# Optimization experiments

Measured on AMD Instinct MI355X. Metric: run time of the kernel, lower is better.

The kernel has to match this reference:

```python
import jax, jax.numpy as jnp
import numpy as np

NUM_HEADS = 16


def setup_inputs() -> dict:
    key = jax.random.key(0)
    ks = jax.random.split(key, 8)
    S, B, E, L, P = 512, 32, 1024, 16, 10
    query = jax.random.normal(ks[0], (S, B, E), dtype=jnp.float32)
    prompt_ids = jax.random.randint(ks[1], (B, 1), 0, P, dtype=jnp.int32)
    batch_weight = jax.random.uniform(ks[2], (B,), dtype=jnp.float32)
    # xavier_uniform-like init for in_proj_weight
    bound = float(np.sqrt(6.0 / (3 * E + E)))
    in_proj_weight = jax.random.uniform(ks[3], (3 * E, E), minval=-bound, maxval=bound, dtype=jnp.float32)
    in_proj_bias = jnp.zeros((3 * E,), dtype=jnp.float32)
    ob = float(np.sqrt(6.0 / (E + E)))
    out_proj_weight = jax.random.uniform(ks[4], (E, E), minval=-ob, maxval=ob, dtype=jnp.float32)
    out_proj_bias = jnp.zeros((E,), dtype=jnp.float32)
    # prefix_pool: K-half uniform(-1,1), V-half zeros (as in torch init)
    pk = jax.random.uniform(ks[5], (P, 1, L, E), minval=-1.0, maxval=1.0, dtype=jnp.float32)
    prefix_pool = jnp.concatenate([pk, jnp.zeros((P, 1, L, E), dtype=jnp.float32)], axis=1)
    return {
        "query": query,
        "prompt_ids": prompt_ids,
        "batch_weight": batch_weight,
        "in_proj_weight": in_proj_weight,
        "in_proj_bias": in_proj_bias,
        "out_proj_weight": out_proj_weight,
        "out_proj_bias": out_proj_bias,
        "prefix_pool": prefix_pool,
    }


def _sdpa(q, k, v, scale):
    # q: [B,H,S,D], k/v: [B,H,T,D]
    scores = jnp.einsum("bhsd,bhtd->bhst", q, k) * scale
    probs = jax.nn.softmax(scores, axis=-1)
    return jnp.einsum("bhst,bhtd->bhsd", probs, v)


def reference(query, prompt_ids, batch_weight, in_proj_weight, in_proj_bias,
              out_proj_weight, out_proj_bias, prefix_pool):
    S, B, E = query.shape
    H = NUM_HEADS
    D = E // H
    scale = 1.0 / jnp.sqrt(jnp.asarray(D, dtype=query.dtype))

    # packed in-projection (q is k is v)
    qkv = query @ in_proj_weight.T + in_proj_bias          # [S,B,3E]
    q, k, v = jnp.split(qkv, 3, axis=-1)
    to_bhsd = lambda t: t.reshape(S, B, H, D).transpose(1, 2, 0, 3)  # [B,H,S,D]
    q, k, v = to_bhsd(q), to_bhsd(k), to_bhsd(v)

    # main attention
    attn = _sdpa(q, k, v, scale)                           # [B,H,S,D]

    # prefix attention
    prefix = prefix_pool[prompt_ids[:, 0]]                 # [B,2,L,E]
    L = prefix.shape[2]
    pk = prefix[:, 0].reshape(B, L, H, D).transpose(0, 2, 1, 3)  # [B,H,L,D]
    pv = prefix[:, 1].reshape(B, L, H, D).transpose(0, 2, 1, 3)
    attn_prefix = _sdpa(q, pk, pv, scale)                  # [B,H,S,D]
    attn_prefix = attn_prefix * batch_weight[:, None, None, None]

    out = attn + attn_prefix
    out = out.transpose(2, 0, 1, 3).reshape(S, B, E)       # [S,B,E]
    out = out @ out_proj_weight.T + out_proj_bias
    return out
```

## Files before the change

### kernel.cpp

```cpp
#include <hip/hip_runtime.h>
#include <stdint.h>

typedef unsigned short u16;
typedef __attribute__((ext_vector_type(8))) __bf16 bf16x8;
typedef __attribute__((ext_vector_type(4))) float f32x4;
typedef __attribute__((ext_vector_type(8))) unsigned short ushort8;

__device__ __forceinline__ u16 f2bf(float f) {
  unsigned int u = __builtin_bit_cast(unsigned int, f);
  return (u16)((u + 0x7fffu + ((u >> 16) & 1u)) >> 16);
}

__device__ __forceinline__ float fexp2(float x) {
  float r;
  asm volatile("v_exp_f32 %0, %1" : "=v"(r) : "v"(x));
  return r;
}

__device__ __forceinline__ f32x4 mfma16(bf16x8 a, bf16x8 b, f32x4 c) {
  return __builtin_amdgcn_mfma_f32_16x16x32_bf16(a, b, c, 0, 0, 0);
}

__device__ __forceinline__ void gload_lds16(const void* g, void* l) {
  __builtin_amdgcn_global_load_lds((const __attribute__((address_space(1))) void*)g,
                                   (__attribute__((address_space(3))) void*)l,
                                   16, 0, 0);
}

#define KSCALE 0.18033688011112294f

__global__ void __launch_bounds__(256) cvt_all(
    const float* __restrict__ q, const float* __restrict__ w1,
    const float* __restrict__ w2, u16* __restrict__ qb,
    u16* __restrict__ w1b, u16* __restrict__ w2b) {
  int i = blockIdx.x * 256 + threadIdx.x;
  const float* src;
  u16* dst;
  int off;
  if (i < 4194304) {
    src = q; dst = qb; off = i;
  } else if (i < 4194304 + 786432) {
    src = w1; dst = w1b; off = i - 4194304;
  } else {
    src = w2; dst = w2b; off = i - 4980736;
  }
  float4 v = ((const float4*)src)[off];
  u16* d = dst + (size_t)off * 4;
  d[0] = f2bf(v.x); d[1] = f2bf(v.y); d[2] = f2bf(v.z); d[3] = f2bf(v.w);
}

#define LDV(p) (*(const bf16x8*)(p))
#define RD_LO(AS, C) { aL[0]=LDV(AS+aRow+(C)); aL[1]=LDV(AS+aRow+1024+(C)); \
                       aL[2]=LDV(AS+aRow+2048+(C)); aL[3]=LDV(AS+aRow+3072+(C)); }
#define RD_HI(AS, C) { aH[0]=LDV(AS+aRow+4096+(C)); aH[1]=LDV(AS+aRow+5120+(C)); \
                       aH[2]=LDV(AS+aRow+6144+(C)); aH[3]=LDV(AS+aRow+7168+(C)); }
#define RD_B(BS, R, C) { R[0]=LDV(BS+bRow+(C)); R[1]=LDV(BS+bRow+1024+(C)); \
                         R[2]=LDV(BS+bRow+2048+(C)); R[3]=LDV(BS+bRow+3072+(C)); }
#define STA(DST, Q, T) gload_lds16(baseA + (Q)*K64 + (size_t)(T)*64, (DST) + (Q)*4096 + stDst)
#define STB(DST, Q, T) gload_lds16(baseB + (Q)*K64 + (size_t)(T)*64, (DST) + (Q)*4096 + stDst)
#define MM_LO(BB) { _Pragma("unroll") for (int mi=0;mi<4;++mi) \
                    _Pragma("unroll") for (int ni=0;ni<4;++ni) \
                      acc[mi][ni]=mfma16(aL[mi],(BB)[ni],acc[mi][ni]); }
#define MM_HI(BB) { _Pragma("unroll") for (int mi=0;mi<4;++mi) \
                    _Pragma("unroll") for (int ni=0;ni<4;++ni) \
                      acc[mi+4][ni]=mfma16(aH[mi],(BB)[ni],acc[mi+4][ni]); }
#define VMW(N) asm volatile("s_waitcnt vmcnt(" #N ")" ::: "memory")
#define BAR() __builtin_amdgcn_s_barrier()
#define PRIO1() __builtin_amdgcn_s_setprio(1)
#define PRIO0() __builtin_amdgcn_s_setprio(0)
#define MFMA_PH(MM, BB) { PRIO1(); MM(BB); PRIO0(); }

template <int MODE>
__global__ void __launch_bounds__(512, 2) gemm8p(
    const u16* __restrict__ A, const u16* __restrict__ B,
    const float* __restrict__ bias, void* __restrict__ Cout,
    u16* __restrict__ q_out, u16* __restrict__ k_out, u16* __restrict__ v_out,
    int M, int N, int K) {
  __shared__ alignas(16) u16 SH[65536];

  const int tid = threadIdx.x;
  const int w = tid >> 6, l = tid & 63;
  const int wm = w >> 2, wn = w & 3;
  const long bm = (long)blockIdx.x * 256;
  const long bn = (long)blockIdx.y * 256;
  const int NT = K >> 6;
  const int NIT = NT >> 1;

  const int srow = w * 8 + (l >> 3);
  const int schk = ((l & 7) ^ (l >> 3)) * 8;
  const u16* baseA = A + (bm + srow) * (size_t)K + schk;
  const u16* baseB = B + (bn + srow) * (size_t)K + schk;
  const size_t K64 = (size_t)K * 64;
  const int stDst = w * 512;

  u16* const as0 = SH;
  u16* const as1 = SH + 16384;
  u16* const bs0 = SH + 32768;
  u16* const bs1 = SH + 49152;

  const int fr = l & 15, fkg = l >> 4;
  const int sw = (fr & 7) << 3;
  const int c0 = (fkg * 8) ^ sw;
  const int c1 = (32 + fkg * 8) ^ sw;
  const int aRow = (wm * 128 + fr) * 64;
  const int bRow = (wn * 64 + fr) * 64;

  f32x4 acc[8][4] = {};
  bf16x8 aL[4], aH[4], b0[4], b1[4];

  STB(bs0, 0, 0); STB(bs0, 1, 0); STB(bs0, 2, 0); STB(bs0, 3, 0);
  STA(as0, 0, 0); STA(as0, 1, 0); STA(as0, 2, 0); STA(as0, 3, 0);
  STB(bs1, 0, 1); STB(bs1, 1, 1);
  VMW(2); BAR();
  RD_LO(as0, c0); RD_B(bs0, b0, c0);

  for (int it = 0; it < NIT - 1; ++it) {
    const int t1 = 2 * it + 1, t2 = 2 * it + 2, t3 = 2 * it + 3;
    STA(as1, 0, t1); STA(as1, 2, t1); STA(as1, 1, t1); STA(as1, 3, t1);
    STB(bs1, 2, t1); STB(bs1, 3, t1);
    RD_HI(as0, c0);
    MFMA_PH(MM_LO, b0); BAR();
    RD_LO(as0, c1); RD_B(bs0, b1, c1);
    MFMA_PH(MM_HI, b0); BAR();
    STB(bs0, 0, t2); STB(bs0, 1, t2); STB(bs0, 2, t2); STB(bs0, 3, t2);
    VMW(4);
    RD_HI(as0, c1);
    MFMA_PH(MM_LO, b1); BAR();
    STA(as0, 0, t2); STA(as0, 2, t2);
    RD_LO(as1, c0); RD_B(bs1, b0, c0);
    MFMA_PH(MM_HI, b1); BAR();
    STA(as0, 1, t2); STA(as0, 3, t2);
    RD_HI(as1, c0);
    MFMA_PH(MM_LO, b0); BAR();
    RD_LO(as1, c1); RD_B(bs1, b1, c1);
    MFMA_PH(MM_HI, b0); BAR();
    STB(bs1, 0, t3); STB(bs1, 1, t3);
    VMW(2);
    RD_HI(as1, c1);
    MFMA_PH(MM_LO, b1); BAR();
    RD_LO(as0, c0); RD_B(bs0, b0, c0);
    MFMA_PH(MM_HI, b1); BAR();
  }

  {
    const int t1 = NT - 1;
    STA(as1, 0, t1); STA(as1, 2, t1); STA(as1, 1, t1); STA(as1, 3, t1);
    STB(bs1, 2, t1); STB(bs1, 3, t1);
    RD_HI(as0, c0);
    MFMA_PH(MM_LO, b0); BAR();
    RD_LO(as0, c1); RD_B(bs0, b1, c1);
    MFMA_PH(MM_HI, b0); BAR();
    VMW(0);
    RD_HI(as0, c1);
    MFMA_PH(MM_LO, b1); BAR();
    RD_LO(as1, c0); RD_B(bs1, b0, c0);
    MFMA_PH(MM_HI, b1); BAR();
    RD_HI(as1, c0);
    MFMA_PH(MM_LO, b0); BAR();
    RD_LO(as1, c1); RD_B(bs1, b1, c1);
    MFMA_PH(MM_HI, b0); BAR();
    RD_HI(as1, c1);
    MFMA_PH(MM_LO, b1); BAR();
    MFMA_PH(MM_HI, b1);
    BAR();
  }

  if (MODE == 0) {
    const int r0 = wm * 128 + ((l >> 4) << 2);
    const int cc0 = wn * 64 + (l & 15);
#pragma unroll
    for (int mi = 0; mi < 8; ++mi) {
#pragma unroll
      for (int j = 0; j < 4; ++j) {
        long r = bm + r0 + mi * 16 + j;
#pragma unroll
        for (int ni = 0; ni < 4; ++ni) {
          long c = bn + cc0 + ni * 16;
          ((float*)Cout)[r * N + c] = acc[mi][ni][j] + bias[c];
        }
      }
    }
  } else {
    const int sec = (int)(bn >> 10);
    const float kmul = (sec == 0) ? KSCALE : 1.0f;
    const int colBase = wn * 64 + (l & 15);
    const int rowBase = wm * 128 + ((l >> 4) << 2);
#pragma unroll
    for (int mi = 0; mi < 8; ++mi) {
#pragma unroll
      for (int j = 0; j < 4; ++j) {
        int row = rowBase + mi * 16 + j;
        int rsw = ((row >> 1) & 7) << 3;
#pragma unroll
        for (int ni = 0; ni < 4; ++ni) {
          int col = colBase + ni * 16;
          float v = (acc[mi][ni][j] + bias[bn + col]) * kmul;
          SH[row * 256 + (col ^ rsw)] = f2bf(v);
        }
      }
    }
    __syncthreads();
    u16* const dst = (sec == 0) ? q_out : (sec == 1) ? k_out : v_out;
    const int ebase = (int)(bn & 1023);
#pragma unroll
    for (int k = 0; k < 16; ++k) {
      int s5 = tid + 512 * k;
      int row = s5 >> 5;
      int col = (s5 & 31) * 8;
      ushort8 v = *(const ushort8*)(SH + row * 256 + (col ^ (((row >> 1) & 7) << 3)));
      long r = bm + row;
      int s = (int)(r >> 5), bb = (int)(r & 31);
      int e = ebase + col;
      int hh = e >> 6, d0 = e & 63;
      *(ushort8*)(dst + (((size_t)(bb * 16 + hh) * 512 + s) * 64) + d0) = v;
    }
  }
}

__global__ void __launch_bounds__(1024, 4) attn_v4(
    const u16* __restrict__ Q, const u16* __restrict__ K, const u16* __restrict__ V,
    const float* __restrict__ prefix_pool, const int* __restrict__ prompt_ids,
    const float* __restrict__ batch_weight, u16* __restrict__ attn_out) {
  constexpr int E = 1024, L = 16;
  const int h = blockIdx.x, b = blockIdx.y;
  const int tid = threadIdx.x;
  const int wid = tid >> 6, lane = tid & 63;
  const int fr = lane & 15, fkg = lane >> 4;

  __shared__ alignas(16) u16 Ks[64 * 64];
  __shared__ alignas(16) u16 VTs[64 * 64];
  __shared__ alignas(16) u16 Ps[16][16 * 64];
  __shared__ alignas(16) u16 pKs[L * 64];
  __shared__ alignas(16) u16 pVTs[64 * 32];

  const size_t bh = (size_t)(b * 16 + h);
  const u16* Kbase = K + bh * 512 * 64;
  const u16* Vbase = V + bh * 512 * 64;
  const u16* Qbase = Q + bh * 512 * 64;
  const int q0 = wid * 32;

  const bool isK = (tid < 512);
  const int st = isK ? tid : tid - 512;
  const int srow = st >> 3;
  const int scol = (st & 7) * 8;
  const u16* sbase = (isK ? Kbase : Vbase) + srow * 64 + scol;

  ushort8 stgA, stgB;
  stgA = *(const ushort8*)(sbase);

  const int pid = prompt_ids[b];
  const float* pk = prefix_pool + ((size_t)pid * 2 * L) * E + h * 64;
  const float* pv = pk + (size_t)L * E;
  if (tid < 256) {
    int ll = tid >> 4, d0 = (tid & 15) * 4;
    float4 v = *(const float4*)(pk + (size_t)ll * E + d0);
    u16 t4[4] = {f2bf(v.x), f2bf(v.y), f2bf(v.z), f2bf(v.w)};
#pragma unroll
    for (int i = 0; i < 4; ++i)
      pKs[(ll * 64 + d0 + i) ^ ((ll & 7) << 3)] = t4[i];
  } else if (tid < 512) {
    int t = tid - 256;
    int d = t >> 2, kv0 = (t & 3) * 8;
#pragma unroll
    for (int i = 0; i < 8; ++i) {
      int kv = kv0 + i;
      float v = (kv < L) ? pv[(size_t)kv * E + d] : 0.f;
      pVTs[d * 32 + kv] = f2bf(v);
    }
  }

  bf16x8 qf[2][2];
#pragma unroll
  for (int mt = 0; mt < 2; ++mt) {
    int qrow = q0 + mt * 16 + fr;
    qf[mt][0] = *(const bf16x8*)(Qbase + qrow * 64 + fkg * 8);
    qf[mt][1] = *(const bf16x8*)(Qbase + qrow * 64 + 32 + fkg * 8);
  }

  float m2[2] = {-3e38f, -3e38f}, lsum[2] = {0.f, 0.f};
  f32x4 oacc[2][4] = {};
  u16* const pw = Ps[wid];
  const int psw = (fr & 7) << 3;

#define STAGE_WRITE(STG)                                                      \
  if (isK) {                                                                  \
    int e = (srow * 64 + scol) ^ ((srow & 7) << 3);                           \
    *(ushort8*)(Ks + e) = STG;                                                \
  } else {                                                                    \
    _Pragma("unroll") for (int i = 0; i < 8; ++i) {                           \
      int d = scol + i;                                                       \
      VTs[(d * 64 + srow) ^ ((d & 7) << 3)] = STG[i];                         \
    }                                                                         \
  }

#define COMPUTE(CC)                                                           \
  _Pragma("unroll") for (int mt = 0; mt < 2; ++mt) {                          \
    f32x4 sa[4];                                                              \
    _Pragma("unroll") for (int nt = 0; nt < 4; ++nt) {                        \
      int krow = nt * 16 + fr;                                                \
      int kb = krow * 64, swz = (krow & 7) << 3;                              \
      bf16x8 kf0 = *(const bf16x8*)(Ks + ((kb + fkg * 8) ^ swz));             \
      bf16x8 kf1 = *(const bf16x8*)(Ks + ((kb + 32 + fkg * 8) ^ swz));        \
      f32x4 z = {};                                                           \
      sa[nt] = mfma16(kf0, qf[mt][0], z);                                     \
      sa[nt] = mfma16(kf1, qf[mt][1], sa[nt]);                                \
    }                                                                         \
    float mx = sa[0][0];                                                      \
    _Pragma("unroll") for (int nt = 0; nt < 4; ++nt)                          \
      _Pragma("unroll") for (int j = 0; j < 4; ++j)                           \
        mx = fmaxf(mx, sa[nt][j]);                                            \
    mx = fmaxf(mx, __shfl_xor(mx, 16, 64));                                   \
    mx = fmaxf(mx, __shfl_xor(mx, 32, 64));                                   \
    if (!__all(mx <= m2[mt] + 8.0f)) {                                        \
      float mnew = fmaxf(m2[mt], mx);                                         \
      float al = fexp2(m2[mt] - mnew);                                        \
      lsum[mt] *= al;                                                         \
      _Pragma("unroll") for (int j = 0; j < 4; ++j) {                         \
        float alj = __shfl(al, fkg * 4 + j, 64);                              \
        _Pragma("unroll") for (int t = 0; t < 4; ++t) oacc[mt][t][j] *= alj;  \
      }                                                                       \
      m2[mt] = mnew;                                                          \
    }                                                                         \
    float sum = 0.f;                                                          \
    _Pragma("unroll") for (int nt = 0; nt < 4; ++nt)                          \
      _Pragma("unroll") for (int j = 0; j < 4; ++j) {                         \
        float p = fexp2(sa[nt][j] - m2[mt]);                                  \
        sa[nt][j] = p;                                                        \
        sum += p;                                                             \
      }                                                                       \
    sum += __shfl_xor(sum, 16, 64);                                           \
    sum += __shfl_xor(sum, 32, 64);                                           \
    lsum[mt] += sum;                                                          \
    _Pragma("unroll") for (int nt = 0; nt < 4; ++nt)                          \
      _Pragma("unroll") for (int i = 0; i < 2; ++i) {                         \
        unsigned int pack = (unsigned int)f2bf(sa[nt][2 * i]) |               \
                            ((unsigned int)f2bf(sa[nt][2 * i + 1]) << 16);    \
        int kv = nt * 16 + fkg * 4 + 2 * i;                                   \
        *(unsigned int*)(pw + fr * 64 + (kv ^ psw)) = pack;                   \
      }                                                                       \
    _Pragma("unroll") for (int kk = 0; kk < 2; ++kk) {                        \
      bf16x8 pa = *(const bf16x8*)(pw + fr * 64 + ((kk * 32 + fkg * 8) ^ psw)); \
      _Pragma("unroll") for (int t = 0; t < 4; ++t) {                         \
        int vd = t * 16 + fr;                                                 \
        bf16x8 vf = *(const bf16x8*)(VTs + ((vd * 64 + kk * 32 + fkg * 8) ^ ((vd & 7) << 3))); \
        oacc[mt][t] = mfma16(pa, vf, oacc[mt][t]);                            \
      }                                                                       \
    }                                                                         \
  }

#define CHUNK(CUR, NXT, C)                                                    \
  {                                                                           \
    STAGE_WRITE(CUR);                                                         \
    if ((C) < 7) NXT = *(const ushort8*)(sbase + ((C) + 1) * 4096);           \
    __syncthreads();                                                          \
    COMPUTE(C);                                                               \
    __syncthreads();                                                          \
  }

  CHUNK(stgA, stgB, 0);
  CHUNK(stgB, stgA, 1);
  CHUNK(stgA, stgB, 2);
  CHUNK(stgB, stgA, 3);
  CHUNK(stgA, stgB, 4);
  CHUNK(stgB, stgA, 5);
  CHUNK(stgA, stgB, 6);
  CHUNK(stgB, stgA, 7);

  const float bw = batch_weight[b];
#pragma unroll
  for (int mt = 0; mt < 2; ++mt) {
    f32x4 sp;
    {
      int swz = (fr & 7) << 3;
      bf16x8 a0 = *(const bf16x8*)(pKs + ((fr * 64 + fkg * 8) ^ swz));
      bf16x8 a1 = *(const bf16x8*)(pKs + ((fr * 64 + 32 + fkg * 8) ^ swz));
      f32x4 z = {};
      sp = mfma16(a0, qf[mt][0], z);
      sp = mfma16(a1, qf[mt][1], sp);
    }
    float mx = fmaxf(fmaxf(sp[0], sp[1]), fmaxf(sp[2], sp[3]));
    mx = fmaxf(mx, __shfl_xor(mx, 16, 64));
    mx = fmaxf(mx, __shfl_xor(mx, 32, 64));
    float psum = 0.f;
#pragma unroll
    for (int j = 0; j < 4; ++j) {
      float p = fexp2(sp[j] - mx);
      sp[j] = p;
      psum += p;
    }
    psum += __shfl_xor(psum, 16, 64);
    psum += __shfl_xor(psum, 32, 64);
#pragma unroll
    for (int i = 0; i < 2; ++i) {
      unsigned int pack = (unsigned int)f2bf(sp[2 * i]) |
                          ((unsigned int)f2bf(sp[2 * i + 1]) << 16);
      int kv = fkg * 4 + 2 * i;
      *(unsigned int*)(pw + fr * 64 + (kv ^ psw)) = pack;
      int kv2 = 16 + fkg * 4 + 2 * i;
      *(unsigned int*)(pw + fr * 64 + (kv2 ^ psw)) = 0u;
    }
    f32x4 op[4] = {};
    {
      bf16x8 pa = *(const bf16x8*)(pw + fr * 64 + ((fkg * 8) ^ psw));
#pragma unroll
      for (int t = 0; t < 4; ++t) {
        bf16x8 vf = *(const bf16x8*)(pVTs + (t * 16 + fr) * 32 + fkg * 8);
        op[t] = mfma16(pa, vf, op[t]);
      }
    }
#pragma unroll
    for (int j = 0; j < 4; ++j) {
      float lj = __shfl(lsum[mt], fkg * 4 + j, 64);
      float lpj = __shfl(psum, fkg * 4 + j, 64);
      int s = q0 + mt * 16 + fkg * 4 + j;
      size_t m = (size_t)s * 32 + b;
      float invl = 1.f / lj, invlp = 1.f / lpj;
#pragma unroll
      for (int t = 0; t < 4; ++t) {
        float v = oacc[mt][t][j] * invl + bw * op[t][j] * invlp;
        attn_out[m * E + h * 64 + t * 16 + fr] = f2bf(v);
      }
    }
  }
}

extern "C" void kernel_launch(void* const* d_in, const int* in_sizes, int n_in,
                              void* d_out, int out_size, void* d_ws, size_t ws_size,
                              hipStream_t stream) {
  const float* query = (const float*)d_in[0];
  const int* prompt_ids = (const int*)d_in[1];
  const float* batch_weight = (const float*)d_in[2];
  const float* in_proj_w = (const float*)d_in[3];
  const float* in_proj_b = (const float*)d_in[4];
  const float* out_proj_w = (const float*)d_in[5];
  const float* out_proj_b = (const float*)d_in[6];
  const float* prefix_pool = (const float*)d_in[7];
  float* out = (float*)d_out;

  u16* qbf = (u16*)d_ws;
  u16* wqkv = qbf + (size_t)16384 * 1024;
  u16* wout = wqkv + (size_t)3072 * 1024;
  u16* qx = wout + (size_t)1024 * 1024;
  u16* kx = qx + (size_t)32 * 16 * 512 * 64;
  u16* vx = kx + (size_t)32 * 16 * 512 * 64;
  u16* attnb = vx + (size_t)32 * 16 * 512 * 64;

  cvt_all<<<20480, 256, 0, stream>>>(query, in_proj_w, out_proj_w,
                                     qbf, wqkv, wout);

  gemm8p<2><<<dim3(64, 12), 512, 0, stream>>>(qbf, wqkv, in_proj_b, nullptr,
                                              qx, kx, vx, 16384, 3072, 1024);
  attn_v4<<<dim3(16, 32), 1024, 0, stream>>>(qx, kx, vx, prefix_pool, prompt_ids,
                                             batch_weight, attnb);
  gemm8p<0><<<dim3(64, 4), 512, 0, stream>>>(attnb, wout, out_proj_b, out,
                                             nullptr, nullptr, nullptr,
                                             16384, 1024, 1024);
}
```

Measured before the change: 250.1 us.

## Halve attention block to 512 threads with 64 query rows per wave

The attention kernel now launches 512 threads per block, and each wave handles 64 query rows (4 m-tiles) instead of 32. K and V fragments are loaded from LDS once per chunk into registers and reused across all four m-tiles. Each thread stages twice as much K/V data. This cuts LDS read traffic and barrier cost per query row, at the price of much higher register pressure (oacc 4x4, kf/vf arrays) and fewer waves for latency hiding.

```diff
diff --git a/kernel.cpp b/kernel.cpp
--- a/kernel.cpp
+++ b/kernel.cpp
@@ -141,7 +141,6 @@
     RD_LO(as0, c0); RD_B(bs0, b0, c0);
     MFMA_PH(MM_HI, b1); BAR();
   }
-
   {
     const int t1 = NT - 1;
     STA(as1, 0, t1); STA(as1, 2, t1); STA(as1, 1, t1); STA(as1, 3, t1);
@@ -217,7 +216,7 @@
   }
 }
 
-__global__ void __launch_bounds__(1024, 4) attn_v4(
+__global__ void __launch_bounds__(512, 4) attn_v5(
     const u16* __restrict__ Q, const u16* __restrict__ K, const u16* __restrict__ V,
     const float* __restrict__ prefix_pool, const int* __restrict__ prompt_ids,
     const float* __restrict__ batch_weight, u16* __restrict__ attn_out) {
@@ -229,7 +228,7 @@
 
   __shared__ alignas(16) u16 Ks[64 * 64];
   __shared__ alignas(16) u16 VTs[64 * 64];
-  __shared__ alignas(16) u16 Ps[16][16 * 64];
+  __shared__ alignas(16) u16 Ps[8][16 * 64];
   __shared__ alignas(16) u16 pKs[L * 64];
   __shared__ alignas(16) u16 pVTs[64 * 32];
 
@@ -237,16 +236,17 @@
   const u16* Kbase = K + bh * 512 * 64;
   const u16* Vbase = V + bh * 512 * 64;
   const u16* Qbase = Q + bh * 512 * 64;
-  const int q0 = wid * 32;
-
-  const bool isK = (tid < 512);
-  const int st = isK ? tid : tid - 512;
-  const int srow = st >> 3;
-  const int scol = (st & 7) * 8;
-  const u16* sbase = (isK ? Kbase : Vbase) + srow * 64 + scol;
-
-  ushort8 stgA, stgB;
-  stgA = *(const ushort8*)(sbase);
+  const int q0 = wid * 64;
+
+  const bool isK = (tid < 256);
+  const int st = tid & 255;
+  const int srow = st >> 2;
+  const int sc16 = (st & 3) * 16;
+  const u16* sbase = (isK ? Kbase : Vbase) + srow * 64 + sc16;
+
+  ushort8 cA = *(const ushort8*)(sbase);
+  ushort8 cB = *(const ushort8*)(sbase + 8);
+  ushort8 nA, nB;
 
   const int pid = prompt_ids[b];
   const float* pk = prefix_pool + ((size_t)pid * 2 * L) * E + h * 64;
@@ -258,7 +258,7 @@
 #pragma unroll
     for (int i = 0; i < 4; ++i)
       pKs[(ll * 64 + d0 + i) ^ ((ll & 7) << 3)] = t4[i];
-  } else if (tid < 512) {
+  } else {
     int t = tid - 256;
     int d = t >> 2, kv0 = (t & 3) * 8;
 #pragma unroll
@@ -269,106 +269,123 @@
     }
   }
 
-  bf16x8 qf[2][2];
-#pragma unroll
-  for (int mt = 0; mt < 2; ++mt) {
+  bf16x8 qf[4][2];
+#pragma unroll
+  for (int mt = 0; mt < 4; ++mt) {
     int qrow = q0 + mt * 16 + fr;
     qf[mt][0] = *(const bf16x8*)(Qbase + qrow * 64 + fkg * 8);
     qf[mt][1] = *(const bf16x8*)(Qbase + qrow * 64 + 32 + fkg * 8);
   }
 
-  float m2[2] = {-3e38f, -3e38f}, lsum[2] = {0.f, 0.f};
-  f32x4 oacc[2][4] = {};
+  float m2[4] = {-3e38f, -3e38f, -3e38f, -3e38f};
+  float lsum[4] = {0.f, 0.f, 0.f, 0.f};
+  f32x4 oacc[4][4] = {};
   u16* const pw = Ps[wid];
   const int psw = (fr & 7) << 3;
 
-#define STAGE_WRITE(STG)                                                      \
+#define STAGE_WR(RA, RB)                                                      \
   if (isK) {                                                                  \
-    int e = (srow * 64 + scol) ^ ((srow & 7) << 3);                           \
-    *(ushort8*)(Ks + e) = STG;                                                \
+    int swz = (srow & 7) << 3;                                                \
+    *(ushort8*)(Ks + ((srow * 64 + sc16) ^ swz)) = RA;                        \
+    *(ushort8*)(Ks + ((srow * 64 + sc16 + 8) ^ swz)) = RB;                    \
   } else {                                                                    \
     _Pragma("unroll") for (int i = 0; i < 8; ++i) {                           \
-      int d = scol + i;                                                       \
-      VTs[(d * 64 + srow) ^ ((d & 7) << 3)] = STG[i];                         \
-    }                                                                         \
-  }
-
-#define COMPUTE(CC)                                                           \
-  _Pragma("unroll") for (int mt = 0; mt < 2; ++mt) {                          \
-    f32x4 sa[4];                                                              \
+      int d = sc16 + i;                                                       \
+      VTs[(d * 64 + srow) ^ ((d & 7) << 3)] = RA[i];                          \
+    }                                                                         \
+    _Pragma("unroll") for (int i = 0; i < 8; ++i) {                           \
+      int d = sc16 + 8 + i;                                                   \
+      VTs[(d * 64 + srow) ^ ((d & 7) << 3)] = RB[i];                          \
+    }                                                                         \
+  }
+
+#define COMPUTE()                                                             \
+  {                                                                           \
+    bf16x8 kf[8], vf[8];                                                      \
     _Pragma("unroll") for (int nt = 0; nt < 4; ++nt) {                        \
       int krow = nt * 16 + fr;                                                \
       int kb = krow * 64, swz = (krow & 7) << 3;                              \
-      bf16x8 kf0 = *(const bf16x8*)(Ks + ((kb + fkg * 8) ^ swz));             \
-      bf16x8 kf1 = *(const bf16x8*)(Ks + ((kb + 32 + fkg * 8) ^ swz));        \
-      f32x4 z = {};                                                           \
-      sa[nt] = mfma16(kf0, qf[mt][0], z);                                     \
-      sa[nt] = mfma16(kf1, qf[mt][1], sa[nt]);                                \
-    }                                                                         \
-    float mx = sa[0][0];                                                      \
-    _Pragma("unroll") for (int nt = 0; nt < 4; ++nt)                          \
-      _Pragma("unroll") for (int j = 0; j < 4; ++j)                           \
-        mx = fmaxf(mx, sa[nt][j]);                                            \
-    mx = fmaxf(mx, __shfl_xor(mx, 16, 64));                                   \
-    mx = fmaxf(mx, __shfl_xor(mx, 32, 64));                                   \
-    if (!__all(mx <= m2[mt] + 8.0f)) {                                        \
-      float mnew = fmaxf(m2[mt], mx);                                         \
-      float al = fexp2(m2[mt] - mnew);                                        \
-      lsum[mt] *= al;                                                         \
-      _Pragma("unroll") for (int j = 0; j < 4; ++j) {                         \
-        float alj = __shfl(al, fkg * 4 + j, 64);                              \
-        _Pragma("unroll") for (int t = 0; t < 4; ++t) oacc[mt][t][j] *= alj;  \
+      kf[nt * 2] = *(const bf16x8*)(Ks + ((kb + fkg * 8) ^ swz));             \
+      kf[nt * 2 + 1] = *(const bf16x8*)(Ks + ((kb + 32 + fkg * 8) ^ swz));    \
+    }                                                                         \
+    _Pragma("unroll") for (int t = 0; t < 4; ++t) {                           \
+      int vd = t * 16 + fr;                                                   \
+      int vb = vd * 64, vsw = (vd & 7) << 3;                                  \
+      vf[t * 2] = *(const bf16x8*)(VTs + ((vb + fkg * 8) ^ vsw));             \
+      vf[t * 2 + 1] = *(const bf16x8*)(VTs + ((vb + 32 + fkg * 8) ^ vsw));    \
+    }                                                                         \
+    _Pragma("unroll") for (int mt = 0; mt < 4; ++mt) {                        \
+      f32x4 sa[4];                                                            \
+      _Pragma("unroll") for (int nt = 0; nt < 4; ++nt) {                      \
+        f32x4 z = {};                                                         \
+        sa[nt] = mfma16(kf[nt * 2], qf[mt][0], z);                            \
+        sa[nt] = mfma16(kf[nt * 2 + 1], qf[mt][1], sa[nt]);                   \
       }                                                                       \
-      m2[mt] = mnew;                                                          \
-    }                                                                         \
-    float sum = 0.f;                                                          \
-    _Pragma("unroll") for (int nt = 0; nt < 4; ++nt)                          \
-      _Pragma("unroll") for (int j = 0; j < 4; ++j) {                         \
-        float p = fexp2(sa[nt][j] - m2[mt]);                                  \
-        sa[nt][j] = p;                                                        \
-        sum += p;                                                             \
+      float mx = sa[0][0];                                                    \
+      _Pragma("unroll") for (int nt = 0; nt < 4; ++nt)                        \
+        _Pragma("unroll") for (int j = 0; j < 4; ++j)                         \
+          mx = fmaxf(mx, sa[nt][j]);                                          \
+      mx = fmaxf(mx, __shfl_xor(mx, 16, 64));                                 \
+      mx = fmaxf(mx, __shfl_xor(mx, 32, 64));                                 \
+      if (!__all(mx <= m2[mt] + 8.0f)) {                                      \
+        float mnew = fmaxf(m2[mt], mx);                                       \
+        float al = fexp2(m2[mt] - mnew);                                      \
+        lsum[mt] *= al;                                                       \
+        _Pragma("unroll") for (int j = 0; j < 4; ++j) {                       \
+          float alj = __shfl(al, fkg * 4 + j, 64);                            \
+          _Pragma("unroll") for (int t = 0; t < 4; ++t) oacc[mt][t][j] *= alj;\
+        }                                                                     \
+        m2[mt] = mnew;                                                        \
       }                                                                       \
-    sum += __shfl_xor(sum, 16, 64);                                           \
-    sum += __shfl_xor(sum, 32, 64);                                           \
-    lsum[mt] += sum;                                                          \
-    _Pragma("unroll") for (int nt = 0; nt < 4; ++nt)                          \
-      _Pragma("unroll") for (int i = 0; i < 2; ++i) {                         \
-        unsigned int pack = (unsigned int)f2bf(sa[nt][2 * i]) |               \
-                            ((unsigned int)f2bf(sa[nt][2 * i + 1]) << 16);    \
-        int kv = nt * 16 + fkg * 4 + 2 * i;                                   \
-        *(unsigned int*)(pw + fr * 64 + (kv ^ psw)) = pack;                   \
+      float sum = 0.f;                                                        \
+      _Pragma("unroll") for (int nt = 0; nt < 4; ++nt)                        \
+        _Pragma("unroll") for (int j = 0; j < 4; ++j) {                       \
+          float p = fexp2(sa[nt][j] - m2[mt]);                                \
+          sa[nt][j] = p;                                                      \
+          sum += p;                                                           \
+        }                                                                     \
+      sum += __shfl_xor(sum, 16, 64);                                         \
+      sum += __shfl_xor(sum, 32, 64);                                         \
+      lsum[mt] += sum;                                                        \
+      _Pragma("unroll") for (int nt = 0; nt < 4; ++nt)                        \
+        _Pragma("unroll") for (int i = 0; i < 2; ++i) {                       \
+          unsigned int pack = (unsigned int)f2bf(sa[nt][2 * i]) |             \
+                              ((unsigned int)f2bf(sa[nt][2 * i + 1]) << 16);  \
+          int kv = nt * 16 + fkg * 4 + 2 * i;                                 \
+          *(unsigned int*)(pw + fr * 64 + (kv ^ psw)) = pack;                 \
+        }                                                                     \
+      _Pragma("unroll") for (int kk = 0; kk < 2; ++kk) {                      \
+        bf16x8 pa = *(const bf16x8*)(pw + fr * 64 + ((kk * 32 + fkg * 8) ^ psw)); \
+        _Pragma("unroll") for (int t = 0; t < 4; ++t)                         \
+          oacc[mt][t] = mfma16(pa, vf[t * 2 + kk], oacc[mt][t]);              \
       }                                                                       \
-    _Pragma("unroll") for (int kk = 0; kk < 2; ++kk) {                        \
-      bf16x8 pa = *(const bf16x8*)(pw + fr * 64 + ((kk * 32 + fkg * 8) ^ psw)); \
-      _Pragma("unroll") for (int t = 0; t < 4; ++t) {                         \
-        int vd = t * 16 + fr;                                                 \
-        bf16x8 vf = *(const bf16x8*)(VTs + ((vd * 64 + kk * 32 + fkg * 8) ^ ((vd & 7) << 3))); \
-        oacc[mt][t] = mfma16(pa, vf, oacc[mt][t]);                            \
-      }                                                                       \
-    }                                                                         \
-  }
-
-#define CHUNK(CUR, NXT, C)                                                    \
+    }                                                                         \
+  }
+
+#define CHUNK2(CA, CB, NA, NB, C)                                             \
   {                                                                           \
-    STAGE_WRITE(CUR);                                                         \
-    if ((C) < 7) NXT = *(const ushort8*)(sbase + ((C) + 1) * 4096);           \
+    STAGE_WR(CA, CB);                                                         \
+    if ((C) < 7) {                                                            \
+      NA = *(const ushort8*)(sbase + ((C) + 1) * 4096);                       \
+      NB = *(const ushort8*)(sbase + ((C) + 1) * 4096 + 8);                   \
+    }                                                                         \
     __syncthreads();                                                          \
-    COMPUTE(C);                                                               \
+    COMPUTE();                                                                \
     __syncthreads();                                                          \
   }
 
-  CHUNK(stgA, stgB, 0);
-  CHUNK(stgB, stgA, 1);
-  CHUNK(stgA, stgB, 2);
-  CHUNK(stgB, stgA, 3);
-  CHUNK(stgA, stgB, 4);
-  CHUNK(stgB, stgA, 5);
-  CHUNK(stgA, stgB, 6);
-  CHUNK(stgB, stgA, 7);
+  CHUNK2(cA, cB, nA, nB, 0);
+  CHUNK2(nA, nB, cA, cB, 1);
+  CHUNK2(cA, cB, nA, nB, 2);
+  CHUNK2(nA, nB, cA, cB, 3);
+  CHUNK2(cA, cB, nA, nB, 4);
+  CHUNK2(nA, nB, cA, cB, 5);
+  CHUNK2(cA, cB, nA, nB, 6);
+  CHUNK2(nA, nB, cA, cB, 7);
 
   const float bw = batch_weight[b];
 #pragma unroll
-  for (int mt = 0; mt < 2; ++mt) {
+  for (int mt = 0; mt < 4; ++mt) {
     f32x4 sp;
     {
       int swz = (fr & 7) << 3;
@@ -404,8 +421,8 @@
       bf16x8 pa = *(const bf16x8*)(pw + fr * 64 + ((fkg * 8) ^ psw));
 #pragma unroll
       for (int t = 0; t < 4; ++t) {
-        bf16x8 vf = *(const bf16x8*)(pVTs + (t * 16 + fr) * 32 + fkg * 8);
-        op[t] = mfma16(pa, vf, op[t]);
+        bf16x8 vfp = *(const bf16x8*)(pVTs + (t * 16 + fr) * 32 + fkg * 8);
+        op[t] = mfma16(pa, vfp, op[t]);
       }
     }
 #pragma unroll
@@ -450,8 +467,8 @@
 
   gemm8p<2><<<dim3(64, 12), 512, 0, stream>>>(qbf, wqkv, in_proj_b, nullptr,
                                               qx, kx, vx, 16384, 3072, 1024);
-  attn_v4<<<dim3(16, 32), 1024, 0, stream>>>(qx, kx, vx, prefix_pool, prompt_ids,
-                                             batch_weight, attnb);
+  attn_v5<<<dim3(16, 32), 512, 0, stream>>>(qx, kx, vx, prefix_pool, prompt_ids,
+                                            batch_weight, attnb);
   gemm8p<0><<<dim3(64, 4), 512, 0, stream>>>(attnb, wout, out_proj_b, out,
                                              nullptr, nullptr, nullptr,
                                              16384, 1024, 1024);
```

Result: slower. 535.3 us (+114.0%).
